# Kernel tuning notes

Hardware: AMD Instinct MI355X
Metric: run time of the kernel (lower is better)

## Reference

```python
import jax, jax.numpy as jnp
import numpy as np

NDIR = 5    # directions (hardcoded range(5) in torch forward)
E = 16      # num_experts
W = 3       # local_window (neighbors per expert, includes self)
D = 128     # expert_dim
P = 256     # patches per expert (equal-size partition of num_patches)
B = 4       # batch
DEPTH = 8   # cantor_depth


def _cantor_coord(pos, max_len, depth):
    x = pos / max(1, max_len - 1)
    x = max(1e-06, min(x, 1.0 - 1e-06))
    val, factor = 0.0, 0.5
    for _ in range(depth):
        x *= 3.0
        digit = int(x)
        x -= digit
        if digit == 2:
            val += factor
        factor *= 0.5
    return val

# Static routing table (buffer in the torch module): W nearest experts by
# |cantor coord| distance; neighbor projections are visited in ascending
# expert-id order in the torch loop, hence the sort.
_coords = np.array([_cantor_coord(i, E, DEPTH) for i in range(E)], dtype=np.float32)
_routes = np.zeros((E, W), dtype=np.int32)
for _i in range(E):
    _d = np.abs(_coords - _coords[_i])
    _routes[_i] = np.sort(np.argsort(_d, kind='stable')[:W])
ROUTES = jnp.asarray(_routes)  # [E, W]


def setup_inputs() -> dict:
    key = jax.random.key(0)
    k1, k2, k3, k4 = jax.random.split(key, 4)
    return {
        'Q_aff': jax.random.normal(k1, (NDIR, E, B, P), jnp.float32),
        'K_aff': jax.random.normal(k2, (NDIR, E, B, P), jnp.float32),
        'V': jax.random.normal(k3, (NDIR, E, B, P, D), jnp.float32),
        'betas': jax.random.normal(k4, (E, E), jnp.float32),
        'temperature': jnp.ones((1,), jnp.float32),
        'fusion_weights': jnp.ones((NDIR,), jnp.float32) / NDIR,
    }


def reference(Q_aff, K_aff, V, betas, temperature, fusion_weights):
    routes = ROUTES                                   # [E, W]
    # Gather neighbor K affinities / values per expert (replaces pad/stack loop).
    K_n = K_aff[:, routes]                            # [NDIR, E, W, B, P]
    V_n = V[:, routes]                                # [NDIR, E, W, B, P, D]
    K_nb = jnp.transpose(K_n, (0, 1, 3, 2, 4))        # [NDIR, E, B, W, P]
    temp = jnp.abs(temperature[0]) + 1e-06
    # scores[x,e,b,p,w,q] = Q[x,e,b,p] * K_neighbor[x,e,b,w,q] / temp
    scores = Q_aff[:, :, :, :, None, None] * K_nb[:, :, :, None, :, :] / temp
    # Cross-expert edges are scaled by sigmoid(beta); self edges are not.
    is_self = routes == jnp.arange(E)[:, None]        # [E, W]
    beta_fac = jnp.where(is_self, 1.0,
                         jax.nn.sigmoid(betas[jnp.arange(E)[:, None], routes]))
    scores = scores * beta_fac[None, :, None, None, :, None]
    attn = jax.nn.softmax(scores.reshape(NDIR, E, B, P, W * P), axis=-1)
    V_flat = jnp.transpose(V_n, (0, 1, 3, 2, 4, 5)).reshape(NDIR, E, B, W * P, D)
    attended = jnp.einsum('xebpk,xebkf->xebpf', attn, V_flat)  # [NDIR,E,B,P,D]
    # Expert e owns contiguous patches [e*P, (e+1)*P) -> scatter is a reshape.
    attended = jnp.transpose(attended, (0, 2, 1, 3, 4)).reshape(NDIR, B, E * P, D)
    wts = jax.nn.softmax(fusion_weights)
    return jnp.einsum('x,xbnf->bnf', wts, attended)   # [B, E*P, D]
```

## Files before the change

### kernel.cpp

```cpp
#include <hip/hip_runtime.h>
#include <math.h>

#define NDIR 5
#define E_ 16
#define W_ 3
#define D_ 128
#define P_ 256
#define B_ 4
#define ROWS 64
#define NPQ 4
#define STEPS 24

typedef __attribute__((ext_vector_type(8))) short short8;
typedef __attribute__((ext_vector_type(4))) float f32x4;
typedef __attribute__((ext_vector_type(8))) float f32x8;

struct RoutesArg { int r[E_][W_]; };

static RoutesArg make_routes() {
    float coords[E_];
    for (int i = 0; i < E_; ++i) {
        double x = (double)i / (double)(E_ - 1);
        if (x < 1e-6) x = 1e-6;
        if (x > 1.0 - 1e-6) x = 1.0 - 1e-6;
        double val = 0.0, factor = 0.5;
        for (int d = 0; d < 8; ++d) {
            x *= 3.0;
            int digit = (int)x;
            x -= (double)digit;
            if (digit == 2) val += factor;
            factor *= 0.5;
        }
        coords[i] = (float)val;
    }
    RoutesArg R;
    for (int i = 0; i < E_; ++i) {
        float d[E_]; int idx[E_];
        for (int j = 0; j < E_; ++j) { d[j] = fabsf(coords[j] - coords[i]); idx[j] = j; }
        for (int a = 1; a < E_; ++a) {
            int key = idx[a]; float kd = d[key];
            int c = a - 1;
            while (c >= 0 && d[idx[c]] > kd) { idx[c + 1] = idx[c]; --c; }
            idx[c + 1] = key;
        }
        int top[W_] = { idx[0], idx[1], idx[2] };
        if (top[0] > top[1]) { int t = top[0]; top[0] = top[1]; top[1] = t; }
        if (top[1] > top[2]) { int t = top[1]; top[1] = top[2]; top[2] = t; }
        if (top[0] > top[1]) { int t = top[0]; top[0] = top[1]; top[1] = t; }
        for (int w = 0; w < W_; ++w) R.r[i][w] = top[w];
    }
    return R;
}

static __device__ __forceinline__ unsigned int cvt_pk_bf16(float lo, float hi) {
    unsigned int r;
    asm("v_cvt_pk_bf16_f32 %0, %1, %2" : "=v"(r) : "v"(lo), "v"(hi));
    return r;
}

static __device__ __forceinline__ short8 pack8(f32x8 a) {
    union { unsigned int u[4]; short8 s; } cv;
    cv.u[0] = cvt_pk_bf16(a[0], a[1]);
    cv.u[1] = cvt_pk_bf16(a[2], a[3]);
    cv.u[2] = cvt_pk_bf16(a[4], a[5]);
    cv.u[3] = cvt_pk_bf16(a[6], a[7]);
    return cv.s;
}

template <bool ATOMIC>
__global__ __launch_bounds__(256, 4) void cantor_partial_kernel(
    const float* __restrict__ Q, const float* __restrict__ K,
    const float* __restrict__ V, const float* __restrict__ betas,
    const float* __restrict__ temperature, const float* __restrict__ fusion,
    float* __restrict__ target, RoutesArg routes)
{
    __shared__ float s_lds[W_ * P_];

    const int orig = blockIdx.x;
    const int wg   = (orig & 7) * 160 + (orig >> 3);

    const int pq = wg & 3;
    const int b  = (wg >> 2) & 3;
    const int e  = (wg >> 4) & 15;
    const int x  = wg >> 8;

    const int tid  = threadIdx.x;
    const int lane = tid & 63;
    const int wv   = tid >> 6;
    const int l15  = lane & 15;
    const int lg   = lane >> 4;

    const int rowbase = (wv >> 1) * 32;
    const int f0      = (wv & 1) * 64;

    const float temp = fabsf(temperature[0]) + 1e-6f;

    float fwx;
    {
        float fv[NDIR], fmx = -1e30f, fsum = 0.f;
        #pragma unroll
        for (int i = 0; i < NDIR; ++i) { fv[i] = fusion[i]; fmx = fmaxf(fmx, fv[i]); }
        #pragma unroll
        for (int i = 0; i < NDIR; ++i) { fv[i] = __expf(fv[i] - fmx); fsum += fv[i]; }
        fwx = fv[x] / fsum;
    }

    int rt[W_]; float bf3[W_];
    #pragma unroll
    for (int w = 0; w < W_; ++w) {
        rt[w] = routes.r[e][w];
        float bv_ = betas[e * E_ + rt[w]];
        bf3[w] = (rt[w] == e) ? 1.0f : 1.0f / (1.0f + __expf(-bv_));
    }

    #pragma unroll
    for (int w = 0; w < W_; ++w)
        s_lds[w * P_ + tid] =
            K[(((size_t)(x * E_ + rt[w])) * B_ + b) * P_ + tid] * bf3[w];

    const float* Qb = Q + (((size_t)(x * E_ + e)) * B_ + b) * P_ + pq * ROWS + rowbase;
    float q2[2];
    q2[0] = Qb[l15] / temp;
    q2[1] = Qb[16 + l15] / temp;

    const float* vb0 = V + (((size_t)(x * E_ + rt[0])) * B_ + b) * (size_t)(P_ * D_) + f0 + l15;
    const float* vb1 = V + (((size_t)(x * E_ + rt[1])) * B_ + b) * (size_t)(P_ * D_) + f0 + l15;
    const float* vb2 = V + (((size_t)(x * E_ + rt[2])) * B_ + b) * (size_t)(P_ * D_) + f0 + l15;
    const float* sp0 = s_lds + 0 * P_ + 8 * lg;
    const float* sp1 = s_lds + 1 * P_ + 8 * lg;
    const float* sp2 = s_lds + 2 * P_ + 8 * lg;

    __syncthreads();

    f32x4 acc[2][4];
    #pragma unroll
    for (int fr = 0; fr < 2; ++fr)
        #pragma unroll
        for (int c = 0; c < 4; ++c)
            acc[fr][c] = (f32x4){0.f, 0.f, 0.f, 0.f};
    float den[2] = {0.f, 0.f};

    f32x8 hA0, hA1, hB0, hB1;

    #define VPTR(g) ((((g) < 8) ? vb0 : (((g) < 16) ? vb1 : vb2)) \
                     + (size_t)((((g) & 7) * 32) + 8 * lg) * D_)
    #define SPTR(g) ((((g) < 8) ? sp0 : (((g) < 16) ? sp1 : sp2)) + (((g) & 7) * 32))

    #define LOADH(d0, d1, vp_, cbase) do {                    \
        _Pragma("unroll")                                     \
        for (int i_ = 0; i_ < 8; ++i_) {                      \
            d0[i_] = (vp_)[i_ * D_ + (cbase) * 16];           \
            d1[i_] = (vp_)[i_ * D_ + ((cbase) + 1) * 16];     \
        }                                                     \
    } while (0)

    {
        const float* vp0 = VPTR(0);
        LOADH(hA0, hA1, vp0, 0);
    }

    for (int g = 0; g < STEPS; ++g) {
        const float* vpg = VPTR(g);
        LOADH(hB0, hB1, vpg, 2);

        const float* sp = SPTR(g);
        f32x8 sv;
        {
            const float4 s0_ = *reinterpret_cast<const float4*>(sp);
            const float4 s1_ = *reinterpret_cast<const float4*>(sp + 4);
            sv[0] = s0_.x; sv[1] = s0_.y; sv[2] = s0_.z; sv[3] = s0_.w;
            sv[4] = s1_.x; sv[5] = s1_.y; sv[6] = s1_.z; sv[7] = s1_.w;
        }
        short8 af[2];
        #pragma unroll
        for (int fr = 0; fr < 2; ++fr) {
            f32x8 ev;
            #pragma unroll
            for (int i = 0; i < 8; ++i) ev[i] = __expf(q2[fr] * sv[i]);
            den[fr] += ((ev[0] + ev[1]) + (ev[2] + ev[3])) +
                       ((ev[4] + ev[5]) + (ev[6] + ev[7]));
            af[fr] = pack8(ev);
        }

        {
            const short8 b0 = pack8(hA0);
            const short8 b1 = pack8(hA1);
            acc[0][0] = __builtin_amdgcn_mfma_f32_16x16x32_bf16(af[0], b0, acc[0][0], 0, 0, 0);
            acc[1][0] = __builtin_amdgcn_mfma_f32_16x16x32_bf16(af[1], b0, acc[1][0], 0, 0, 0);
            acc[0][1] = __builtin_amdgcn_mfma_f32_16x16x32_bf16(af[0], b1, acc[0][1], 0, 0, 0);
            acc[1][1] = __builtin_amdgcn_mfma_f32_16x16x32_bf16(af[1], b1, acc[1][1], 0, 0, 0);
        }

        if (g + 1 < STEPS) {
            const float* vpn = VPTR(g + 1);
            LOADH(hA0, hA1, vpn, 0);
        }

        {
            const short8 b2 = pack8(hB0);
            const short8 b3 = pack8(hB1);
            acc[0][2] = __builtin_amdgcn_mfma_f32_16x16x32_bf16(af[0], b2, acc[0][2], 0, 0, 0);
            acc[1][2] = __builtin_amdgcn_mfma_f32_16x16x32_bf16(af[1], b2, acc[1][2], 0, 0, 0);
            acc[0][3] = __builtin_amdgcn_mfma_f32_16x16x32_bf16(af[0], b3, acc[0][3], 0, 0, 0);
            acc[1][3] = __builtin_amdgcn_mfma_f32_16x16x32_bf16(af[1], b3, acc[1][3], 0, 0, 0);
        }
    }
    #undef VPTR
    #undef SPTR
    #undef LOADH

    #pragma unroll
    for (int fr = 0; fr < 2; ++fr) {
        den[fr] += __shfl_xor(den[fr], 16);
        den[fr] += __shfl_xor(den[fr], 32);
    }

    const size_t obase = ((((size_t)b * E_ + e) * NPQ) + pq) * (ROWS * D_);
    float* __restrict__ tgt = ATOMIC
        ? target
        : target + (size_t)x * ((size_t)B_ * E_ * NPQ * ROWS * D_);

    #pragma unroll
    for (int fr = 0; fr < 2; ++fr) {
        #pragma unroll
        for (int r = 0; r < 4; ++r) {
            const float dr = __shfl(den[fr], 4 * lg + r);
            const float sc = fwx / dr;
            const int row = rowbase + fr * 16 + 4 * lg + r;
            float* op = tgt + obase + (size_t)row * D_ + f0;
            #pragma unroll
            for (int c = 0; c < 4; ++c) {
                const float v = sc * acc[fr][c][r];
                if (ATOMIC) atomicAdd(op + c * 16 + l15, v);
                else        op[c * 16 + l15] = v;
            }
        }
    }
}

__global__ __launch_bounds__(256) void reduce5_kernel(
    const float* __restrict__ part, float* __restrict__ out)
{
    const size_t i = (size_t)blockIdx.x * 256 + threadIdx.x;
    const float4* __restrict__ p = reinterpret_cast<const float4*>(part);
    float4 a = p[i];
    #pragma unroll
    for (int x = 1; x < NDIR; ++x) {
        float4 t = p[(size_t)x * 524288 + i];
        a.x += t.x; a.y += t.y; a.z += t.z; a.w += t.w;
    }
    reinterpret_cast<float4*>(out)[i] = a;
}

extern "C" void kernel_launch(void* const* d_in, const int* in_sizes, int n_in,
                              void* d_out, int out_size, void* d_ws, size_t ws_size,
                              hipStream_t stream) {
    (void)in_sizes; (void)n_in;
    RoutesArg R = make_routes();
    const float* Q     = (const float*)d_in[0];
    const float* K     = (const float*)d_in[1];
    const float* V     = (const float*)d_in[2];
    const float* betas = (const float*)d_in[3];
    const float* tempr = (const float*)d_in[4];
    const float* fuse  = (const float*)d_in[5];
    float* out = (float*)d_out;

    const size_t partial_bytes = (size_t)NDIR * B_ * E_ * NPQ * ROWS * D_ * 4;
    dim3 grid(NDIR * E_ * B_ * NPQ);
    dim3 block(256);

    if (ws_size >= partial_bytes) {
        float* part = (float*)d_ws;
        hipLaunchKernelGGL((cantor_partial_kernel<false>), grid, block, 0, stream,
                           Q, K, V, betas, tempr, fuse, part, R);
        hipLaunchKernelGGL(reduce5_kernel, dim3(2048), block, 0, stream,
                           part, out);
    } else {
        (void)hipMemsetAsync(d_out, 0, (size_t)out_size * 4, stream);
        hipLaunchKernelGGL((cantor_partial_kernel<true>), grid, block, 0, stream,
                           Q, K, V, betas, tempr, fuse, out, R);
    }
}
```

Before: 64.88 us.

## Pre-transpose V to bf16 feature-major layout and widen per-wave feature tile

```diff
diff --git a/kernel.cpp b/kernel.cpp
--- a/kernel.cpp
+++ b/kernel.cpp
@@ -52,6 +52,12 @@
     return R;
 }
 
+static __device__ __forceinline__ unsigned short f2bf(float f) {
+    union { float f; unsigned int u; } v; v.f = f;
+    unsigned int r = (v.u + 0x7FFFu + ((v.u >> 16) & 1u)) >> 16;
+    return (unsigned short)r;
+}
+
 static __device__ __forceinline__ unsigned int cvt_pk_bf16(float lo, float hi) {
     unsigned int r;
     asm("v_cvt_pk_bf16_f32 %0, %1, %2" : "=v"(r) : "v"(lo), "v"(hi));
@@ -67,34 +73,207 @@
     return cv.s;
 }
 
+static __device__ __forceinline__ short8 u4_to_s8(uint4 u) {
+    union { uint4 u; short8 s; } cv; cv.u = u; return cv.s;
+}
+
+__global__ __launch_bounds__(256) void vt_prep_kernel(
+    const float* __restrict__ V, unsigned short* __restrict__ Vt)
+{
+    const int sub  = blockIdx.x & 3;
+    const int slab = blockIdx.x >> 2;
+    const int tid  = threadIdx.x;
+    const float4* __restrict__ src =
+        reinterpret_cast<const float4*>(V + (size_t)slab * (P_ * D_));
+    unsigned short* __restrict__ dst = Vt + (size_t)slab * (P_ * D_);
+    #pragma unroll
+    for (int it = 0; it < 8; ++it) {
+        const int idx4 = sub * 2048 + it * 256 + tid;
+        const int k  = idx4 >> 5;
+        const int f4 = (idx4 & 31) * 4;
+        const float4 v = src[idx4];
+        dst[(size_t)(f4 + 0) * P_ + k] = f2bf(v.x);
+        dst[(size_t)(f4 + 1) * P_ + k] = f2bf(v.y);
+        dst[(size_t)(f4 + 2) * P_ + k] = f2bf(v.z);
+        dst[(size_t)(f4 + 3) * P_ + k] = f2bf(v.w);
+    }
+}
+
 template <bool ATOMIC>
-__global__ __launch_bounds__(256, 4) void cantor_partial_kernel(
+__global__ __launch_bounds__(256, 4) void cantor_partial2_kernel(
+    const float* __restrict__ Q, const float* __restrict__ K,
+    const unsigned short* __restrict__ Vt, const float* __restrict__ betas,
+    const float* __restrict__ temperature, const float* __restrict__ fusion,
+    float* __restrict__ target, RoutesArg routes)
+{
+    __shared__ float s_lds[W_ * P_];
+
+    const int orig = blockIdx.x;
+    const int wg   = (orig & 7) * 160 + (orig >> 3);
+
+    const int pq = wg & 3;
+    const int b  = (wg >> 2) & 3;
+    const int e  = (wg >> 4) & 15;
+    const int x  = wg >> 8;
+
+    const int tid  = threadIdx.x;
+    const int lane = tid & 63;
+    const int wv   = tid >> 6;
+    const int l15  = lane & 15;
+    const int lg   = lane >> 4;
+
+    const int rowbase = wv * 16;
+
+    const float temp = fabsf(temperature[0]) + 1e-6f;
+
+    float fwx;
+    {
+        float fv[NDIR], fmx = -1e30f, fsum = 0.f;
+        #pragma unroll
+        for (int i = 0; i < NDIR; ++i) { fv[i] = fusion[i]; fmx = fmaxf(fmx, fv[i]); }
+        #pragma unroll
+        for (int i = 0; i < NDIR; ++i) { fv[i] = __expf(fv[i] - fmx); fsum += fv[i]; }
+        fwx = fv[x] / fsum;
+    }
+
+    int rt[W_]; float bf3[W_];
+    #pragma unroll
+    for (int w = 0; w < W_; ++w) {
+        rt[w] = routes.r[e][w];
+        float bv_ = betas[e * E_ + rt[w]];
+        bf3[w] = (rt[w] == e) ? 1.0f : 1.0f / (1.0f + __expf(-bv_));
+    }
+
+    #pragma unroll
+    for (int w = 0; w < W_; ++w)
+        s_lds[w * P_ + tid] =
+            K[(((size_t)(x * E_ + rt[w])) * B_ + b) * P_ + tid] * bf3[w];
+
+    const float q1 =
+        Q[(((size_t)(x * E_ + e)) * B_ + b) * P_ + pq * ROWS + rowbase + l15] / temp;
+
+    const uint4* vt0 = reinterpret_cast<const uint4*>(Vt)
+        + ((size_t)(x * E_ + rt[0]) * B_ + b) * (P_ * D_ / 8) + l15 * 32 + lg;
+    const uint4* vt1 = reinterpret_cast<const uint4*>(Vt)
+        + ((size_t)(x * E_ + rt[1]) * B_ + b) * (P_ * D_ / 8) + l15 * 32 + lg;
+    const uint4* vt2 = reinterpret_cast<const uint4*>(Vt)
+        + ((size_t)(x * E_ + rt[2]) * B_ + b) * (P_ * D_ / 8) + l15 * 32 + lg;
+    const float* sp0 = s_lds + 0 * P_ + 8 * lg;
+    const float* sp1 = s_lds + 1 * P_ + 8 * lg;
+    const float* sp2 = s_lds + 2 * P_ + 8 * lg;
+
+    __syncthreads();
+
+    f32x4 acc[8];
+    #pragma unroll
+    for (int c = 0; c < 8; ++c) acc[c] = (f32x4){0.f, 0.f, 0.f, 0.f};
+    float den = 0.f;
+
+    #define VTP(g) (((g) < 8 ? vt0 : ((g) < 16 ? vt1 : vt2)) + (((g) & 7) * 4))
+    #define SPTR(g) ((((g) < 8) ? sp0 : (((g) < 16) ? sp1 : sp2)) + (((g) & 7) * 32))
+
+    #define LOADB(B0,B1,B2,B3,B4,B5,B6,B7, g) do {            \
+        const uint4* p_ = VTP(g);                             \
+        B0 = p_[0 * 512]; B1 = p_[1 * 512];                   \
+        B2 = p_[2 * 512]; B3 = p_[3 * 512];                   \
+        B4 = p_[4 * 512]; B5 = p_[5 * 512];                   \
+        B6 = p_[6 * 512]; B7 = p_[7 * 512];                   \
+    } while (0)
+
+    #define AWORK(af_, g) do {                                           \
+        const float* sp_ = SPTR(g);                                      \
+        f32x8 sv_;                                                       \
+        {                                                                \
+            const float4 s0_ = *reinterpret_cast<const float4*>(sp_);    \
+            const float4 s1_ = *reinterpret_cast<const float4*>(sp_ + 4);\
+            sv_[0]=s0_.x; sv_[1]=s0_.y; sv_[2]=s0_.z; sv_[3]=s0_.w;      \
+            sv_[4]=s1_.x; sv_[5]=s1_.y; sv_[6]=s1_.z; sv_[7]=s1_.w;      \
+        }                                                                \
+        f32x8 ev_;                                                       \
+        _Pragma("unroll")                                                \
+        for (int i_ = 0; i_ < 8; ++i_) ev_[i_] = __expf(q1 * sv_[i_]);   \
+        den += ((ev_[0]+ev_[1]) + (ev_[2]+ev_[3])) +                     \
+               ((ev_[4]+ev_[5]) + (ev_[6]+ev_[7]));                      \
+        af_ = pack8(ev_);                                                \
+    } while (0)
+
+    #define MFMA8(B0,B1,B2,B3,B4,B5,B6,B7, af_) do {                                      \
+        acc[0] = __builtin_amdgcn_mfma_f32_16x16x32_bf16(af_, u4_to_s8(B0), acc[0],0,0,0);\
+        acc[1] = __builtin_amdgcn_mfma_f32_16x16x32_bf16(af_, u4_to_s8(B1), acc[1],0,0,0);\
+        acc[2] = __builtin_amdgcn_mfma_f32_16x16x32_bf16(af_, u4_to_s8(B2), acc[2],0,0,0);\
+        acc[3] = __builtin_amdgcn_mfma_f32_16x16x32_bf16(af_, u4_to_s8(B3), acc[3],0,0,0);\
+        acc[4] = __builtin_amdgcn_mfma_f32_16x16x32_bf16(af_, u4_to_s8(B4), acc[4],0,0,0);\
+        acc[5] = __builtin_amdgcn_mfma_f32_16x16x32_bf16(af_, u4_to_s8(B5), acc[5],0,0,0);\
+        acc[6] = __builtin_amdgcn_mfma_f32_16x16x32_bf16(af_, u4_to_s8(B6), acc[6],0,0,0);\
+        acc[7] = __builtin_amdgcn_mfma_f32_16x16x32_bf16(af_, u4_to_s8(B7), acc[7],0,0,0);\
+    } while (0)
+
+    uint4 a0,a1,a2,a3,a4,a5,a6,a7;
+    uint4 b0,b1,b2,b3,b4,b5,b6,b7;
+    short8 af;
+
+    LOADB(a0,a1,a2,a3,a4,a5,a6,a7, 0);
+
+    for (int gp = 0; gp < STEPS / 2; ++gp) {
+        const int g0 = 2 * gp, g1 = 2 * gp + 1;
+        LOADB(b0,b1,b2,b3,b4,b5,b6,b7, g1);
+        AWORK(af, g0);
+        MFMA8(a0,a1,a2,a3,a4,a5,a6,a7, af);
+        if (g1 + 1 < STEPS)
+            LOADB(a0,a1,a2,a3,a4,a5,a6,a7, g1 + 1);
+        AWORK(af, g1);
+        MFMA8(b0,b1,b2,b3,b4,b5,b6,b7, af);
+    }
+    #undef VTP
+    #undef SPTR
+    #undef LOADB
+    #undef AWORK
+    #undef MFMA8
+
+    den += __shfl_xor(den, 16);
+    den += __shfl_xor(den, 32);
+
+    const size_t obase = ((((size_t)b * E_ + e) * NPQ) + pq) * (ROWS * D_);
+    float* __restrict__ tgt = ATOMIC
+        ? target
+        : target + (size_t)x * ((size_t)B_ * E_ * NPQ * ROWS * D_);
+
+    #pragma unroll
+    for (int r = 0; r < 4; ++r) {
+        const float dr = __shfl(den, 4 * lg + r);
+        const float sc = fwx / dr;
+        const int row = rowbase + 4 * lg + r;
+        float* op = tgt + obase + (size_t)row * D_;
+        #pragma unroll
+        for (int c = 0; c < 8; ++c) {
+            const float v = sc * acc[c][r];
+            if (ATOMIC) atomicAdd(op + c * 16 + l15, v);
+            else        op[c * 16 + l15] = v;
+        }
+    }
+}
+
+__global__ __launch_bounds__(256, 4) void cantor_partial_old_kernel(
     const float* __restrict__ Q, const float* __restrict__ K,
     const float* __restrict__ V, const float* __restrict__ betas,
     const float* __restrict__ temperature, const float* __restrict__ fusion,
     float* __restrict__ target, RoutesArg routes)
 {
     __shared__ float s_lds[W_ * P_];
-
     const int orig = blockIdx.x;
     const int wg   = (orig & 7) * 160 + (orig >> 3);
-
     const int pq = wg & 3;
     const int b  = (wg >> 2) & 3;
     const int e  = (wg >> 4) & 15;
     const int x  = wg >> 8;
-
     const int tid  = threadIdx.x;
     const int lane = tid & 63;
     const int wv   = tid >> 6;
     const int l15  = lane & 15;
     const int lg   = lane >> 4;
-
     const int rowbase = (wv >> 1) * 32;
     const int f0      = (wv & 1) * 64;
-
     const float temp = fabsf(temperature[0]) + 1e-6f;
-
     float fwx;
     {
         float fv[NDIR], fmx = -1e30f, fsum = 0.f;
@@ -104,7 +283,6 @@
         for (int i = 0; i < NDIR; ++i) { fv[i] = __expf(fv[i] - fmx); fsum += fv[i]; }
         fwx = fv[x] / fsum;
     }
-
     int rt[W_]; float bf3[W_];
     #pragma unroll
     for (int w = 0; w < W_; ++w) {
@@ -112,26 +290,21 @@
         float bv_ = betas[e * E_ + rt[w]];
         bf3[w] = (rt[w] == e) ? 1.0f : 1.0f / (1.0f + __expf(-bv_));
     }
-
     #pragma unroll
     for (int w = 0; w < W_; ++w)
         s_lds[w * P_ + tid] =
             K[(((size_t)(x * E_ + rt[w])) * B_ + b) * P_ + tid] * bf3[w];
-
     const float* Qb = Q + (((size_t)(x * E_ + e)) * B_ + b) * P_ + pq * ROWS + rowbase;
     float q2[2];
     q2[0] = Qb[l15] / temp;
     q2[1] = Qb[16 + l15] / temp;
-
     const float* vb0 = V + (((size_t)(x * E_ + rt[0])) * B_ + b) * (size_t)(P_ * D_) + f0 + l15;
     const float* vb1 = V + (((size_t)(x * E_ + rt[1])) * B_ + b) * (size_t)(P_ * D_) + f0 + l15;
     const float* vb2 = V + (((size_t)(x * E_ + rt[2])) * B_ + b) * (size_t)(P_ * D_) + f0 + l15;
     const float* sp0 = s_lds + 0 * P_ + 8 * lg;
     const float* sp1 = s_lds + 1 * P_ + 8 * lg;
     const float* sp2 = s_lds + 2 * P_ + 8 * lg;
-
     __syncthreads();
-
     f32x4 acc[2][4];
     #pragma unroll
     for (int fr = 0; fr < 2; ++fr)
@@ -139,13 +312,10 @@
         for (int c = 0; c < 4; ++c)
             acc[fr][c] = (f32x4){0.f, 0.f, 0.f, 0.f};
     float den[2] = {0.f, 0.f};
-
     f32x8 hA0, hA1, hB0, hB1;
-
     #define VPTR(g) ((((g) < 8) ? vb0 : (((g) < 16) ? vb1 : vb2)) \
                      + (size_t)((((g) & 7) * 32) + 8 * lg) * D_)
-    #define SPTR(g) ((((g) < 8) ? sp0 : (((g) < 16) ? sp1 : sp2)) + (((g) & 7) * 32))
-
+    #define SPTRO(g) ((((g) < 8) ? sp0 : (((g) < 16) ? sp1 : sp2)) + (((g) & 7) * 32))
     #define LOADH(d0, d1, vp_, cbase) do {                    \
         _Pragma("unroll")                                     \
         for (int i_ = 0; i_ < 8; ++i_) {                      \
@@ -153,17 +323,14 @@
             d1[i_] = (vp_)[i_ * D_ + ((cbase) + 1) * 16];     \
         }                                                     \
     } while (0)
-
     {
         const float* vp0 = VPTR(0);
         LOADH(hA0, hA1, vp0, 0);
     }
-
     for (int g = 0; g < STEPS; ++g) {
         const float* vpg = VPTR(g);
         LOADH(hB0, hB1, vpg, 2);
-
-        const float* sp = SPTR(g);
+        const float* sp = SPTRO(g);
         f32x8 sv;
         {
             const float4 s0_ = *reinterpret_cast<const float4*>(sp);
@@ -181,45 +348,36 @@
                        ((ev[4] + ev[5]) + (ev[6] + ev[7]));
             af[fr] = pack8(ev);
         }
-
         {
-            const short8 b0 = pack8(hA0);
-            const short8 b1 = pack8(hA1);
-            acc[0][0] = __builtin_amdgcn_mfma_f32_16x16x32_bf16(af[0], b0, acc[0][0], 0, 0, 0);
-            acc[1][0] = __builtin_amdgcn_mfma_f32_16x16x32_bf16(af[1], b0, acc[1][0], 0, 0, 0);
-            acc[0][1] = __builtin_amdgcn_mfma_f32_16x16x32_bf16(af[0], b1, acc[0][1], 0, 0, 0);
-            acc[1][1] = __builtin_amdgcn_mfma_f32_16x16x32_bf16(af[1], b1, acc[1][1], 0, 0, 0);
-        }
-
+            const short8 c0 = pack8(hA0);
+            const short8 c1 = pack8(hA1);
+            acc[0][0] = __builtin_amdgcn_mfma_f32_16x16x32_bf16(af[0], c0, acc[0][0], 0, 0, 0);
+            acc[1][0] = __builtin_amdgcn_mfma_f32_16x16x32_bf16(af[1], c0, acc[1][0], 0, 0, 0);
+            acc[0][1] = __builtin_amdgcn_mfma_f32_16x16x32_bf16(af[0], c1, acc[0][1], 0, 0, 0);
+            acc[1][1] = __builtin_amdgcn_mfma_f32_16x16x32_bf16(af[1], c1, acc[1][1], 0, 0, 0);
+        }
         if (g + 1 < STEPS) {
             const float* vpn = VPTR(g + 1);
             LOADH(hA0, hA1, vpn, 0);
         }
-
         {
-            const short8 b2 = pack8(hB0);
-            const short8 b3 = pack8(hB1);
-            acc[0][2] = __builtin_amdgcn_mfma_f32_16x16x32_bf16(af[0], b2, acc[0][2], 0, 0, 0);
-            acc[1][2] = __builtin_amdgcn_mfma_f32_16x16x32_bf16(af[1], b2, acc[1][2], 0, 0, 0);
-            acc[0][3] = __builtin_amdgcn_mfma_f32_16x16x32_bf16(af[0], b3, acc[0][3], 0, 0, 0);
-            acc[1][3] = __builtin_amdgcn_mfma_f32_16x16x32_bf16(af[1], b3, acc[1][3], 0, 0, 0);
+            const short8 c2 = pack8(hB0);
+            const short8 c3 = pack8(hB1);
+            acc[0][2] = __builtin_amdgcn_mfma_f32_16x16x32_bf16(af[0], c2, acc[0][2], 0, 0, 0);
+            acc[1][2] = __builtin_amdgcn_mfma_f32_16x16x32_bf16(af[1], c2, acc[1][2], 0, 0, 0);
+            acc[0][3] = __builtin_amdgcn_mfma_f32_16x16x32_bf16(af[0], c3, acc[0][3], 0, 0, 0);
+            acc[1][3] = __builtin_amdgcn_mfma_f32_16x16x32_bf16(af[1], c3, acc[1][3], 0, 0, 0);
         }
     }
     #undef VPTR
-    #undef SPTR
+    #undef SPTRO
     #undef LOADH
-
     #pragma unroll
     for (int fr = 0; fr < 2; ++fr) {
         den[fr] += __shfl_xor(den[fr], 16);
         den[fr] += __shfl_xor(den[fr], 32);
     }
-
     const size_t obase = ((((size_t)b * E_ + e) * NPQ) + pq) * (ROWS * D_);
-    float* __restrict__ tgt = ATOMIC
-        ? target
-        : target + (size_t)x * ((size_t)B_ * E_ * NPQ * ROWS * D_);
-
     #pragma unroll
     for (int fr = 0; fr < 2; ++fr) {
         #pragma unroll
@@ -227,13 +385,10 @@
             const float dr = __shfl(den[fr], 4 * lg + r);
             const float sc = fwx / dr;
             const int row = rowbase + fr * 16 + 4 * lg + r;
-            float* op = tgt + obase + (size_t)row * D_ + f0;
+            float* op = target + obase + (size_t)row * D_ + f0;
             #pragma unroll
-            for (int c = 0; c < 4; ++c) {
-                const float v = sc * acc[fr][c][r];
-                if (ATOMIC) atomicAdd(op + c * 16 + l15, v);
-                else        op[c * 16 + l15] = v;
-            }
+            for (int c = 0; c < 4; ++c)
+                atomicAdd(op + c * 16 + l15, sc * acc[fr][c][r]);
         }
     }
 }
@@ -265,19 +420,29 @@
     const float* fuse  = (const float*)d_in[5];
     float* out = (float*)d_out;
 
-    const size_t partial_bytes = (size_t)NDIR * B_ * E_ * NPQ * ROWS * D_ * 4;
+    const size_t vt_bytes   = (size_t)NDIR * E_ * B_ * P_ * D_ * 2;
+    const size_t part_bytes = (size_t)NDIR * B_ * E_ * NPQ * ROWS * D_ * 4;
+
     dim3 grid(NDIR * E_ * B_ * NPQ);
     dim3 block(256);
 
-    if (ws_size >= partial_bytes) {
-        float* part = (float*)d_ws;
-        hipLaunchKernelGGL((cantor_partial_kernel<false>), grid, block, 0, stream,
-                           Q, K, V, betas, tempr, fuse, part, R);
+    if (ws_size >= vt_bytes + part_bytes) {
+        unsigned short* Vt = (unsigned short*)d_ws;
+        float* part = (float*)((char*)d_ws + vt_bytes);
+        hipLaunchKernelGGL(vt_prep_kernel, dim3(1280), block, 0, stream, V, Vt);
+        hipLaunchKernelGGL((cantor_partial2_kernel<false>), grid, block, 0, stream,
+                           Q, K, Vt, betas, tempr, fuse, part, R);
         hipLaunchKernelGGL(reduce5_kernel, dim3(2048), block, 0, stream,
                            part, out);
+    } else if (ws_size >= vt_bytes) {
+        unsigned short* Vt = (unsigned short*)d_ws;
+        (void)hipMemsetAsync(d_out, 0, (size_t)out_size * 4, stream);
+        hipLaunchKernelGGL(vt_prep_kernel, dim3(1280), block, 0, stream, V, Vt);
+        hipLaunchKernelGGL((cantor_partial2_kernel<true>), grid, block, 0, stream,
+                           Q, K, Vt, betas, tempr, fuse, out, R);
     } else {
         (void)hipMemsetAsync(d_out, 0, (size_t)out_size * 4, stream);
-        hipLaunchKernelGGL((cantor_partial_kernel<true>), grid, block, 0, stream,
+        hipLaunchKernelGGL(cantor_partial_old_kernel, grid, block, 0, stream,
                            Q, K, V, betas, tempr, fuse, out, R);
     }
 }
```

Result: slower. 151.5 us (+133.6%).
